# Kernel tuning notes

Measured on AMD Instinct MI355X. Metric: run time of the kernel, lower is better.

Reference implementation:

```python
import jax, jax.numpy as jnp
import numpy as np

B, SQ, SK, DK, DV = 8, 2048, 2048, 256, 256
EPS = 1e-7  # keras.backend.epsilon()


def setup_inputs() -> dict:
    key = jax.random.key(0)
    kq, kk, kv, km = jax.random.split(key, 4)
    query = jax.random.normal(kq, (B, SQ, DK), dtype=jnp.float32)
    k_ = jax.random.normal(kk, (B, SK, DK), dtype=jnp.float32)
    value = jax.random.normal(kv, (B, SK, DV), dtype=jnp.float32)
    mask = jax.random.uniform(km, (B, SK)) > 0.1
    return {"query": query, "key": k_, "value": value, "mask": mask}


def reference(query, key, value, mask):
    d = query.shape[-1]
    # scores: [B, Sq, Sk]
    e = jnp.einsum('bqd,bkd->bqk', query, key) / jnp.sqrt(jnp.asarray(d, query.dtype))
    # original applies exp(e - max) BEFORE masking (non-standard but faithful)
    e = jnp.exp(e - jnp.max(e, axis=-1, keepdims=True))
    q_len, k_len = query.shape[1], key.shape[1]
    causal = (jnp.arange(k_len)[None, :] <= jnp.arange(q_len)[:, None]).astype(query.dtype)
    e = e * causal[None, :, :]                       # history_only mask
    e = e * mask[:, None, :].astype(query.dtype)     # key padding mask
    a = e / (jnp.sum(e, axis=-1, keepdims=True) + EPS)
    return jnp.einsum('bqk,bkv->bqv', a, value)
```

## Files before the change

### kernel.cpp

```cpp
#include <hip/hip_runtime.h>
#include <hip/hip_bf16.h>

#define B_   8
#define SQ_  2048
#define SK_  2048
#define DK_  256
#define DV_  256

#define KT    32
#define PSTR  40
#define TELEM (KT * DK_)

typedef __bf16 bf16x8 __attribute__((ext_vector_type(8)));
typedef float  f32x4  __attribute__((ext_vector_type(4)));

__device__ __forceinline__ void gl_lds16(const void* g, void* l) {
    __builtin_amdgcn_global_load_lds(
        (const __attribute__((address_space(1))) void*)g,
        (__attribute__((address_space(3))) void*)l, 16, 0, 0);
}

__global__ __launch_bounds__(256)
void make_ktiles(const float* __restrict__ K, __bf16* __restrict__ Kt)
{
    const int t = blockIdx.x, b = blockIdx.y;
    __bf16* out = Kt + ((size_t)(b * 64 + t)) * TELEM;
    const float* src = K + ((size_t)(b * SK_ + t * KT)) * DK_;
    #pragma unroll
    for (int it = 0; it < 4; ++it) {
        int ci  = it * 256 + threadIdx.x;
        int dk8 = ci >> 5;
        int key = ci & 31;
        const float* p = src + (size_t)key * DK_ + dk8 * 8;
        float4 f0 = *(const float4*)(p);
        float4 f1 = *(const float4*)(p + 4);
        bf16x8 o;
        o[0] = (__bf16)f0.x; o[1] = (__bf16)f0.y; o[2] = (__bf16)f0.z; o[3] = (__bf16)f0.w;
        o[4] = (__bf16)f1.x; o[5] = (__bf16)f1.y; o[6] = (__bf16)f1.z; o[7] = (__bf16)f1.w;
        *(bf16x8*)(out + (size_t)ci * 8) = o;
    }
}

__global__ __launch_bounds__(256)
void make_vtiles(const float* __restrict__ V, __bf16* __restrict__ Vt)
{
    const int t = blockIdx.x, b = blockIdx.y;
    __bf16* out = Vt + ((size_t)(b * 64 + t)) * TELEM;
    const float* src = V + ((size_t)(b * SK_ + t * KT)) * DV_;
    #pragma unroll
    for (int it = 0; it < 4; ++it) {
        int ci  = it * 256 + threadIdx.x;
        int kc8 = ci >> 8;
        int dv  = ci & 255;
        const float* p = src + (size_t)(kc8 * 8) * DV_ + dv;
        bf16x8 o;
        #pragma unroll
        for (int j = 0; j < 8; ++j)
            o[j] = (__bf16)p[(size_t)j * DV_];
        *(bf16x8*)(out + (size_t)ci * 8) = o;
    }
}

__global__ __launch_bounds__(256, 4)
void attn_fwd(const float* __restrict__ Qg, const __bf16* __restrict__ Kt,
              const __bf16* __restrict__ Vt, const void* __restrict__ Mv,
              __bf16* __restrict__ Opart, float* __restrict__ Lpart,
              int tpc, int slotcap, int nch)
{
    __shared__ __align__(16) __bf16 sK[TELEM];
    __shared__ __align__(16) __bf16 sV[TELEM];
    __shared__ __align__(16) __bf16 sP[4][16 * PSTR];

    const int tid  = threadIdx.x;
    const int wv   = tid >> 6;
    const int lane = tid & 63;
    const int quad = lane >> 4;
    const int l16  = lane & 15;

    const int b = blockIdx.x;
    const int y = (nch - 1) - blockIdx.y;

    int g = 0;
    while ((tpc >> 2) * (g + 1) * (g + 2) <= y) ++g;
    const int rem = y - (tpc >> 2) * g * (g + 1);
    const int jq  = rem / (g + 1);
    const int qb  = g * (tpc >> 1) + jq;
    const int s   = rem - jq * (g + 1);
    const int nt  = 2 * qb + 2;
    const int nc  = g + 1;
    const int t0  = nt * s / nc;
    const int t1  = nt * (s + 1) / nc;

    const int qrow = qb * 64 + wv * 16;

    const unsigned char* Mb = (const unsigned char*)Mv;
    const int*           Mi = (const int*)Mv;
    int nzb = 0;
    {
        const unsigned int* mw = (const unsigned int*)Mv;
        #pragma unroll
        for (int i = 0; i < 32; ++i) {
            unsigned int w = mw[i];
            nzb += ((w & 0x000000ffu) != 0) + ((w & 0x0000ff00u) != 0)
                 + ((w & 0x00ff0000u) != 0) + ((w & 0xff000000u) != 0);
        }
    }
    const bool mask_byte = (nzb > 40);

    bf16x8 qfrag[8];
    {
        const float* qp = Qg + ((size_t)(b * SQ_ + qrow + l16)) * DK_ + quad * 8;
        #pragma unroll
        for (int kt = 0; kt < 8; ++kt) {
            float4 f0 = *(const float4*)(qp + kt * 32);
            float4 f1 = *(const float4*)(qp + kt * 32 + 4);
            bf16x8 q;
            q[0] = (__bf16)f0.x; q[1] = (__bf16)f0.y; q[2] = (__bf16)f0.z; q[3] = (__bf16)f0.w;
            q[4] = (__bf16)f1.x; q[5] = (__bf16)f1.y; q[6] = (__bf16)f1.z; q[7] = (__bf16)f1.w;
            qfrag[kt] = q;
        }
    }

    f32x4 oacc[16];
    #pragma unroll
    for (int v = 0; v < 16; ++v) oacc[v] = (f32x4){0.f, 0.f, 0.f, 0.f};
    float lsum[4] = {0.f, 0.f, 0.f, 0.f};

    const __bf16* Kbase = Kt + (size_t)b * 64 * TELEM;
    const __bf16* Vbase = Vt + (size_t)b * 64 * TELEM;
    const size_t  mbase = (size_t)b * SK_;

    for (int t = t0; t < t1; ++t) {
        __syncthreads();

        const __bf16* kt_g = Kbase + (size_t)t * TELEM;
        const __bf16* vt_g = Vbase + (size_t)t * TELEM;
        #pragma unroll
        for (int r = 0; r < 4; ++r) {
            int ci = r * 256 + tid;
            gl_lds16(kt_g + (size_t)ci * 8, (char*)sK + ci * 16);
        }
        #pragma unroll
        for (int r = 0; r < 4; ++r) {
            int ci = r * 256 + tid;
            gl_lds16(vt_g + (size_t)ci * 8, (char*)sV + ci * 16);
        }
        __syncthreads();

        const int k0 = t * KT;

        f32x4 s0 = {0.f,0.f,0.f,0.f}, s1 = {0.f,0.f,0.f,0.f};
        #pragma unroll
        for (int kt = 0; kt < 8; ++kt) {
            bf16x8 b0 = *(const bf16x8*)&sK[(size_t)((kt * 4 + quad) * 32 + l16)      * 8];
            bf16x8 b1 = *(const bf16x8*)&sK[(size_t)((kt * 4 + quad) * 32 + 16 + l16) * 8];
            s0 = __builtin_amdgcn_mfma_f32_16x16x32_bf16(qfrag[kt], b0, s0, 0, 0, 0);
            s1 = __builtin_amdgcn_mfma_f32_16x16x32_bf16(qfrag[kt], b1, s1, 0, 0, 0);
        }

        #pragma unroll
        for (int nf = 0; nf < 2; ++nf) {
            f32x4 sv = (nf == 0) ? s0 : s1;
            int key = k0 + nf * 16 + l16;
            float mk = mask_byte ? (Mb[mbase + key] ? 1.0f : 0.0f)
                                 : (Mi[mbase + key] ? 1.0f : 0.0f);
            #pragma unroll
            for (int i = 0; i < 4; ++i) {
                int qr = qrow + quad * 4 + i;
                float p = __expf(sv[i] * 0.0625f);
                p = (key <= qr) ? (p * mk) : 0.0f;
                lsum[i] += p;
                sP[wv][(quad * 4 + i) * PSTR + nf * 16 + l16] = (__bf16)p;
            }
        }
        asm volatile("s_waitcnt lgkmcnt(0)" ::: "memory");
        __builtin_amdgcn_wave_barrier();

        {
            bf16x8 pa = *(const bf16x8*)&sP[wv][l16 * PSTR + quad * 8];
            #pragma unroll
            for (int vf = 0; vf < 16; ++vf) {
                bf16x8 bv = *(const bf16x8*)&sV[(size_t)(quad * 256 + vf * 16 + l16) * 8];
                oacc[vf] = __builtin_amdgcn_mfma_f32_16x16x32_bf16(pa, bv, oacc[vf], 0, 0, 0);
            }
        }
    }

    const size_t slot = ((size_t)(b * 32 + qb)) * slotcap + s;
    #pragma unroll
    for (int i = 0; i < 4; ++i) {
        float v = lsum[i];
        v += __shfl_xor(v, 1);
        v += __shfl_xor(v, 2);
        v += __shfl_xor(v, 4);
        v += __shfl_xor(v, 8);
        lsum[i] = v;
    }
    if (l16 == 0) {
        #pragma unroll
        for (int i = 0; i < 4; ++i)
            Lpart[slot * 64 + wv * 16 + quad * 4 + i] = lsum[i];
    }
    __bf16* ob = Opart + slot * (64 * 256);
    #pragma unroll
    for (int vf = 0; vf < 16; ++vf) {
        #pragma unroll
        for (int i = 0; i < 4; ++i)
            ob[(wv * 16 + quad * 4 + i) * 256 + vf * 16 + l16] = (__bf16)oacc[vf][i];
    }
}

__global__ __launch_bounds__(512)
void attn_reduce(const __bf16* __restrict__ Opart, const float* __restrict__ Lpart,
                 float* __restrict__ Og, int tpc, int slotcap)
{
    const int b  = blockIdx.x;
    const int qb = blockIdx.y;
    const int chunks = (2 * qb + 2 + tpc - 1) / tpc;
    const int tid = threadIdx.x;
    const int row = tid >> 3;
    const int cg  = tid & 7;

    const size_t sbase = ((size_t)(b * 32 + qb)) * slotcap;
    float acc[32];
    #pragma unroll
    for (int i = 0; i < 32; ++i) acc[i] = 0.f;
    float ls = 0.f;

    for (int s = 0; s < chunks; ++s) {
        const __bf16* p = Opart + (sbase + s) * (64 * 256) + row * 256 + cg * 32;
        #pragma unroll
        for (int v = 0; v < 4; ++v) {
            bf16x8 x = *(const bf16x8*)(p + v * 8);
            #pragma unroll
            for (int e = 0; e < 8; ++e) acc[v * 8 + e] += (float)x[e];
        }
        ls += Lpart[(sbase + s) * 64 + row];
    }
    const float inv = 1.0f / (ls + 1e-7f);
    float* op = Og + ((size_t)b * SQ_ + qb * 64 + row) * DV_ + cg * 32;
    #pragma unroll
    for (int v = 0; v < 8; ++v) {
        float4 o;
        o.x = acc[v * 4 + 0] * inv; o.y = acc[v * 4 + 1] * inv;
        o.z = acc[v * 4 + 2] * inv; o.w = acc[v * 4 + 3] * inv;
        *(float4*)(op + v * 4) = o;
    }
}

extern "C" void kernel_launch(void* const* d_in, const int* in_sizes, int n_in,
                              void* d_out, int out_size, void* d_ws, size_t ws_size,
                              hipStream_t stream) {
    const float* Q = (const float*)d_in[0];
    const float* K = (const float*)d_in[1];
    const float* V = (const float*)d_in[2];
    const void*  M = d_in[3];
    float* Out = (float*)d_out;

    __bf16* Ktl = (__bf16*)d_ws;
    __bf16* Vtl = Ktl + (size_t)B_ * 64 * TELEM;
    __bf16* Opart = Vtl + (size_t)B_ * 64 * TELEM;

    auto need = [](int slotcap) -> size_t {
        return (size_t)(16 * 1024 * 1024)
             + (size_t)256 * slotcap * 64 * 256 * 2
             + (size_t)256 * slotcap * 64 * 4;
    };
    int tpc, slotcap, nch;
    if      (ws_size >= need(8)) { tpc = 8;  slotcap = 8; nch = 144; }
    else if (ws_size >= need(4)) { tpc = 16; slotcap = 4; nch = 80;  }
    else                         { tpc = 64; slotcap = 1; nch = 32;  }

    float* Lpart = (float*)(Opart + (size_t)256 * slotcap * 64 * 256);

    make_ktiles<<<dim3(64, B_), dim3(256), 0, stream>>>(K, Ktl);
    make_vtiles<<<dim3(64, B_), dim3(256), 0, stream>>>(V, Vtl);

    attn_fwd<<<dim3(B_, nch), dim3(256), 0, stream>>>(Q, Ktl, Vtl, M, Opart, Lpart,
                                                      tpc, slotcap, nch);
    attn_reduce<<<dim3(B_, 32), dim3(512), 0, stream>>>(Opart, Lpart, Out, tpc, slotcap);
}
```

Before: 156.4 us.

## Double-buffer K/V tiles, stage mask in LDS, transpose tiles via shared memory

The attention kernel now keeps two LDS buffers for the K and V tiles. It prefetches the next tile with global_load_lds while computing on the current one, and uses one barrier per iteration instead of two. The per-key padding mask is loaded once per block into shared memory as floats, replacing a global read each tile. The K/V bf16 tile-packing kernels now read coalesced float4 rows into a padded LDS tile before writing the packed layout. The larger LDS footprint lowers launch_bounds occupancy from 4 to 2 blocks. The 256-entry mask buffer assumes each chunk spans at most 8 tiles.

```diff
diff --git a/kernel.cpp b/kernel.cpp
--- a/kernel.cpp
+++ b/kernel.cpp
@@ -10,6 +10,7 @@
 #define KT    32
 #define PSTR  40
 #define TELEM (KT * DK_)
+#define TSTR  260
 
 typedef __bf16 bf16x8 __attribute__((ext_vector_type(8)));
 typedef float  f32x4  __attribute__((ext_vector_type(4)));
@@ -23,20 +24,26 @@
 __global__ __launch_bounds__(256)
 void make_ktiles(const float* __restrict__ K, __bf16* __restrict__ Kt)
 {
+    __shared__ __bf16 sT[KT * TSTR];
     const int t = blockIdx.x, b = blockIdx.y;
+    const int tid = threadIdx.x;
+    const float* src = K + ((size_t)(b * SK_ + t * KT)) * DK_;
     __bf16* out = Kt + ((size_t)(b * 64 + t)) * TELEM;
-    const float* src = K + ((size_t)(b * SK_ + t * KT)) * DK_;
+
+    #pragma unroll
+    for (int it = 0; it < 8; ++it) {
+        int idx = it * 256 + tid;
+        int r = idx >> 6, c4 = idx & 63;
+        float4 f = *(const float4*)(src + (size_t)r * DK_ + c4 * 4);
+        __bf16* d = &sT[r * TSTR + c4 * 4];
+        d[0] = (__bf16)f.x; d[1] = (__bf16)f.y; d[2] = (__bf16)f.z; d[3] = (__bf16)f.w;
+    }
+    __syncthreads();
     #pragma unroll
     for (int it = 0; it < 4; ++it) {
-        int ci  = it * 256 + threadIdx.x;
-        int dk8 = ci >> 5;
-        int key = ci & 31;
-        const float* p = src + (size_t)key * DK_ + dk8 * 8;
-        float4 f0 = *(const float4*)(p);
-        float4 f1 = *(const float4*)(p + 4);
-        bf16x8 o;
-        o[0] = (__bf16)f0.x; o[1] = (__bf16)f0.y; o[2] = (__bf16)f0.z; o[3] = (__bf16)f0.w;
-        o[4] = (__bf16)f1.x; o[5] = (__bf16)f1.y; o[6] = (__bf16)f1.z; o[7] = (__bf16)f1.w;
+        int ci  = it * 256 + tid;
+        int dk8 = ci >> 5, key = ci & 31;
+        bf16x8 o = *(const bf16x8*)&sT[key * TSTR + dk8 * 8];
         *(bf16x8*)(out + (size_t)ci * 8) = o;
     }
 }
@@ -44,32 +51,43 @@
 __global__ __launch_bounds__(256)
 void make_vtiles(const float* __restrict__ V, __bf16* __restrict__ Vt)
 {
+    __shared__ __bf16 sT[KT * TSTR];
     const int t = blockIdx.x, b = blockIdx.y;
+    const int tid = threadIdx.x;
+    const float* src = V + ((size_t)(b * SK_ + t * KT)) * DV_;
     __bf16* out = Vt + ((size_t)(b * 64 + t)) * TELEM;
-    const float* src = V + ((size_t)(b * SK_ + t * KT)) * DV_;
+
+    #pragma unroll
+    for (int it = 0; it < 8; ++it) {
+        int idx = it * 256 + tid;
+        int r = idx >> 6, c4 = idx & 63;
+        float4 f = *(const float4*)(src + (size_t)r * DV_ + c4 * 4);
+        __bf16* d = &sT[r * TSTR + c4 * 4];
+        d[0] = (__bf16)f.x; d[1] = (__bf16)f.y; d[2] = (__bf16)f.z; d[3] = (__bf16)f.w;
+    }
+    __syncthreads();
     #pragma unroll
     for (int it = 0; it < 4; ++it) {
-        int ci  = it * 256 + threadIdx.x;
-        int kc8 = ci >> 8;
-        int dv  = ci & 255;
-        const float* p = src + (size_t)(kc8 * 8) * DV_ + dv;
+        int ci  = it * 256 + tid;
+        int kc8 = ci >> 8, dv = ci & 255;
         bf16x8 o;
         #pragma unroll
         for (int j = 0; j < 8; ++j)
-            o[j] = (__bf16)p[(size_t)j * DV_];
+            o[j] = sT[(kc8 * 8 + j) * TSTR + dv];
         *(bf16x8*)(out + (size_t)ci * 8) = o;
     }
 }
 
-__global__ __launch_bounds__(256, 4)
+__global__ __launch_bounds__(256, 2)
 void attn_fwd(const float* __restrict__ Qg, const __bf16* __restrict__ Kt,
               const __bf16* __restrict__ Vt, const void* __restrict__ Mv,
               __bf16* __restrict__ Opart, float* __restrict__ Lpart,
               int tpc, int slotcap, int nch)
 {
-    __shared__ __align__(16) __bf16 sK[TELEM];
-    __shared__ __align__(16) __bf16 sV[TELEM];
+    __shared__ __align__(16) __bf16 sK[2][TELEM];
+    __shared__ __align__(16) __bf16 sV[2][TELEM];
     __shared__ __align__(16) __bf16 sP[4][16 * PSTR];
+    __shared__ float sMask[256];
 
     const int tid  = threadIdx.x;
     const int wv   = tid >> 6;
@@ -92,6 +110,7 @@
     const int t1  = nt * (s + 1) / nc;
 
     const int qrow = qb * 64 + wv * 16;
+    const int ck0  = t0 * KT;
 
     const unsigned char* Mb = (const unsigned char*)Mv;
     const int*           Mi = (const int*)Mv;
@@ -106,6 +125,14 @@
         }
     }
     const bool mask_byte = (nzb > 40);
+
+    {
+        int key = ck0 + tid;
+        bool in = tid < (t1 - t0) * KT;
+        bool valid = in && (mask_byte ? (Mb[(size_t)b * SK_ + key] != 0)
+                                      : (Mi[(size_t)b * SK_ + key] != 0));
+        sMask[tid] = valid ? 1.0f : 0.0f;
+    }
 
     bf16x8 qfrag[8];
     {
@@ -128,32 +155,36 @@
 
     const __bf16* Kbase = Kt + (size_t)b * 64 * TELEM;
     const __bf16* Vbase = Vt + (size_t)b * 64 * TELEM;
-    const size_t  mbase = (size_t)b * SK_;
-
-    for (int t = t0; t < t1; ++t) {
-        __syncthreads();
-
+
+    auto stage = [&](int buf, int t) {
         const __bf16* kt_g = Kbase + (size_t)t * TELEM;
         const __bf16* vt_g = Vbase + (size_t)t * TELEM;
         #pragma unroll
         for (int r = 0; r < 4; ++r) {
             int ci = r * 256 + tid;
-            gl_lds16(kt_g + (size_t)ci * 8, (char*)sK + ci * 16);
+            gl_lds16(kt_g + (size_t)ci * 8, (char*)&sK[buf][0] + ci * 16);
         }
         #pragma unroll
         for (int r = 0; r < 4; ++r) {
             int ci = r * 256 + tid;
-            gl_lds16(vt_g + (size_t)ci * 8, (char*)sV + ci * 16);
-        }
-        __syncthreads();
+            gl_lds16(vt_g + (size_t)ci * 8, (char*)&sV[buf][0] + ci * 16);
+        }
+    };
+
+    stage(0, t0);
+    __syncthreads();
+
+    for (int t = t0; t < t1; ++t) {
+        const int buf = (t - t0) & 1;
+        if (t + 1 < t1) stage(buf ^ 1, t + 1);
 
         const int k0 = t * KT;
 
         f32x4 s0 = {0.f,0.f,0.f,0.f}, s1 = {0.f,0.f,0.f,0.f};
         #pragma unroll
         for (int kt = 0; kt < 8; ++kt) {
-            bf16x8 b0 = *(const bf16x8*)&sK[(size_t)((kt * 4 + quad) * 32 + l16)      * 8];
-            bf16x8 b1 = *(const bf16x8*)&sK[(size_t)((kt * 4 + quad) * 32 + 16 + l16) * 8];
+            bf16x8 b0 = *(const bf16x8*)&sK[buf][(size_t)((kt * 4 + quad) * 32 + l16)      * 8];
+            bf16x8 b1 = *(const bf16x8*)&sK[buf][(size_t)((kt * 4 + quad) * 32 + 16 + l16) * 8];
             s0 = __builtin_amdgcn_mfma_f32_16x16x32_bf16(qfrag[kt], b0, s0, 0, 0, 0);
             s1 = __builtin_amdgcn_mfma_f32_16x16x32_bf16(qfrag[kt], b1, s1, 0, 0, 0);
         }
@@ -162,8 +193,7 @@
         for (int nf = 0; nf < 2; ++nf) {
             f32x4 sv = (nf == 0) ? s0 : s1;
             int key = k0 + nf * 16 + l16;
-            float mk = mask_byte ? (Mb[mbase + key] ? 1.0f : 0.0f)
-                                 : (Mi[mbase + key] ? 1.0f : 0.0f);
+            float mk = sMask[key - ck0];
             #pragma unroll
             for (int i = 0; i < 4; ++i) {
                 int qr = qrow + quad * 4 + i;
@@ -180,10 +210,11 @@
             bf16x8 pa = *(const bf16x8*)&sP[wv][l16 * PSTR + quad * 8];
             #pragma unroll
             for (int vf = 0; vf < 16; ++vf) {
-                bf16x8 bv = *(const bf16x8*)&sV[(size_t)(quad * 256 + vf * 16 + l16) * 8];
+                bf16x8 bv = *(const bf16x8*)&sV[buf][(size_t)(quad * 256 + vf * 16 + l16) * 8];
                 oacc[vf] = __builtin_amdgcn_mfma_f32_16x16x32_bf16(pa, bv, oacc[vf], 0, 0, 0);
             }
         }
+        __syncthreads();
     }
 
     const size_t slot = ((size_t)(b * 32 + qb)) * slotcap + s;
```

New measurement: 157.0 us. No clear change (+0.4%).
